# Kernel optimization log

Hardware: AMD Instinct MI355X
Metric: run time of the kernel (lower is better)

Reference implementation:

```python
import jax, jax.numpy as jnp
import numpy as np

B, S, DIM, HID = 2, 256, 128, 128
EPS = 1e-5

def _ln(t, w, b):
    mu = jnp.mean(t, axis=-1, keepdims=True)
    var = jnp.mean(jnp.square(t - mu), axis=-1, keepdims=True)
    return (t - mu) * jax.lax.rsqrt(var + EPS) * w + b

def setup_inputs() -> dict:
    key = jax.random.key(0)
    ks = jax.random.split(key, 8)
    sc = 1.0 / np.sqrt(DIM)
    return {
        "x": jax.random.normal(ks[0], (B, S, S, DIM), dtype=jnp.float32),
        "mask": jax.random.uniform(ks[1], (B, S, S), dtype=jnp.float32),
        "norm_w": jnp.ones((DIM,), jnp.float32),
        "norm_b": jnp.zeros((DIM,), jnp.float32),
        "w_left": jax.random.uniform(ks[2], (HID, DIM), jnp.float32, -sc, sc),
        "w_right": jax.random.uniform(ks[3], (HID, DIM), jnp.float32, -sc, sc),
        "w_lg": jax.random.uniform(ks[4], (HID, DIM), jnp.float32, -sc, sc),
        "w_rg": jax.random.uniform(ks[5], (HID, DIM), jnp.float32, -sc, sc),
        "w_og": jax.random.uniform(ks[6], (HID, DIM), jnp.float32, -sc, sc),
        "out_norm_w": jnp.ones((HID,), jnp.float32),
        "out_norm_b": jnp.zeros((HID,), jnp.float32),
        "w_out": jax.random.uniform(ks[7], (DIM, HID), jnp.float32, -1.0 / np.sqrt(HID), 1.0 / np.sqrt(HID)),
    }

def reference(x, mask, norm_w, norm_b, w_left, w_right, w_lg, w_rg, w_og,
              out_norm_w, out_norm_b, w_out):
    xn = _ln(x, norm_w, norm_b)                      # [B,S,S,D]
    m = mask[..., None]                              # [B,S,S,1]
    left = (xn @ w_left.T) * m * jax.nn.sigmoid(xn @ w_lg.T)    # [B,S,S,H]
    right = (xn @ w_right.T) * m * jax.nn.sigmoid(xn @ w_rg.T)  # [B,S,S,H]
    out_gate = jax.nn.sigmoid(xn @ w_og.T)
    # torch: permute to [B,H,S,S], bf16 bmm, permute back -> out[b,i,j,h] = sum_k L[b,i,k,h]*R[b,j,k,h]
    out = jnp.einsum("bikh,bjkh->bijh",
                     left.astype(jnp.bfloat16), right.astype(jnp.bfloat16),
                     preferred_element_type=jnp.float32)
    out = out.astype(jnp.bfloat16).astype(jnp.float32)
    out = _ln(out, out_norm_w, out_norm_b) * out_gate
    return out @ w_out.T                             # [B,S,S,D]
```

## Files before the change

### kernel.cpp

```cpp
#include <hip/hip_runtime.h>


#define SS 256
#define DD 128
#define HH 128

typedef __attribute__((ext_vector_type(8))) short bf16x8;
typedef __attribute__((ext_vector_type(4))) short bf16x4;
typedef __attribute__((ext_vector_type(4))) float f32x4;

__device__ __forceinline__ unsigned short f2b(float f) {
  unsigned u = __builtin_bit_cast(unsigned, f);
  u = (u + 0x7FFFu + ((u >> 16) & 1u)) >> 16;
  return (unsigned short)u;
}
__device__ __forceinline__ float b2f(unsigned short h) {
  return __builtin_bit_cast(float, ((unsigned)h) << 16);
}
__device__ __forceinline__ float sigmoidf_(float x) {
  return 1.0f / (1.0f + expf(-x));
}

__global__ __launch_bounds__(1024) void k_cvt(
    const float* __restrict__ s0, const float* __restrict__ s1,
    const float* __restrict__ s2, const float* __restrict__ s3,
    const float* __restrict__ s4, const float* __restrict__ s5,
    unsigned short* __restrict__ dst)
{
  int m = blockIdx.x >> 2;
  int e4 = (((blockIdx.x & 3) << 10) | threadIdx.x) << 2;
  const float* s = (m == 0) ? s0 : (m == 1) ? s1 : (m == 2) ? s2
                 : (m == 3) ? s3 : (m == 4) ? s4 : s5;
  f32x4 v = *(const f32x4*)(s + e4);
  bf16x4 r;
  #pragma unroll
  for (int i = 0; i < 4; ++i) r[i] = (short)f2b(v[i]);
  *(bf16x4*)(dst + m * 16384 + e4) = r;
}

__global__ __launch_bounds__(256, 4) void k_stage1(
    const float* __restrict__ x, const float* __restrict__ mask,
    const float* __restrict__ nw, const float* __restrict__ nb,
    const unsigned short* __restrict__ wb,
    unsigned short* __restrict__ Lt, unsigned short* __restrict__ Rt,
    unsigned short* __restrict__ og)
{
  __shared__ unsigned short xnS[64][136];
  __shared__ unsigned short oS[128][72];
  __shared__ float maskS[64];

  const int tid  = threadIdx.x;
  const int wave = tid >> 6, lane = tid & 63;
  const int quad = lane >> 4, l16 = lane & 15;
  const int r0 = blockIdx.x * 64;
  const int bq = r0 >> 16, iq = (r0 >> 8) & 255, j0 = r0 & 255;

  if (tid < 64) maskS[tid] = mask[r0 + tid];

  const float w0 = nw[lane], w1 = nw[lane + 64];
  const float b0 = nb[lane], b1 = nb[lane + 64];
  float v0a[16], v1a[16];
  #pragma unroll
  for (int rr = 0; rr < 16; ++rr) {
    const float* xr = x + (size_t)(r0 + wave * 16 + rr) * DD;
    v0a[rr] = xr[lane];
    v1a[rr] = xr[lane + 64];
  }
  #pragma unroll
  for (int rr = 0; rr < 16; ++rr) {
    int r = wave * 16 + rr;
    float v0 = v0a[rr], v1 = v1a[rr];
    float s = v0 + v1;
    #pragma unroll
    for (int o = 32; o; o >>= 1) s += __shfl_xor(s, o);
    float mu = s * (1.0f / 128.0f);
    float d0 = v0 - mu, d1 = v1 - mu;
    float q = d0 * d0 + d1 * d1;
    #pragma unroll
    for (int o = 32; o; o >>= 1) q += __shfl_xor(q, o);
    float rs = rsqrtf(q * (1.0f / 128.0f) + 1e-5f);
    xnS[r][lane]      = f2b(d0 * rs * w0 + b0);
    xnS[r][lane + 64] = f2b(d1 * rs * w1 + b1);
  }
  __syncthreads();

  const int h0 = wave * 32;
  const int jl = quad * 4;

  auto coopStore = [&](unsigned short* dstBase) {
    int h = tid >> 1, half = tid & 1;
    const bf16x8* s = (const bf16x8*)&oS[h][half * 32];
    bf16x8* d = (bf16x8*)(dstBase +
        ((((size_t)bq * 128 + h) * 256 + iq) * 256 + j0 + half * 32));
    d[0] = s[0]; d[1] = s[1]; d[2] = s[2]; d[3] = s[3];
  };

  auto gatedCompute = [&](const unsigned short* __restrict__ Wv,
                          const unsigned short* __restrict__ Wg,
                          f32x4 (&aV)[4][2], f32x4 (&aG)[4][2]) {
    const unsigned short* pv = Wv + (h0 + l16) * 128 + quad * 8;
    const unsigned short* pg = Wg + (h0 + l16) * 128 + quad * 8;
    #pragma unroll
    for (int rt = 0; rt < 4; ++rt)
      #pragma unroll
      for (int n = 0; n < 2; ++n) {
        aV[rt][n] = f32x4{0.f, 0.f, 0.f, 0.f};
        aG[rt][n] = f32x4{0.f, 0.f, 0.f, 0.f};
      }
    bf16x8 bv[2], bg[2], bvn[2], bgn[2];
    #pragma unroll
    for (int n = 0; n < 2; ++n) {
      bv[n] = *(const bf16x8*)(pv + n * 2048);
      bg[n] = *(const bf16x8*)(pg + n * 2048);
    }
    #pragma unroll
    for (int kk = 0; kk < 4; ++kk) {
      if (kk < 3) {
        #pragma unroll
        for (int n = 0; n < 2; ++n) {
          bvn[n] = *(const bf16x8*)(pv + n * 2048 + (kk + 1) * 32);
          bgn[n] = *(const bf16x8*)(pg + n * 2048 + (kk + 1) * 32);
        }
      }
      #pragma unroll
      for (int rt = 0; rt < 4; ++rt) {
        bf16x8 a = *(const bf16x8*)&xnS[rt * 16 + l16][kk * 32 + quad * 8];
        #pragma unroll
        for (int n = 0; n < 2; ++n) {
          aG[rt][n] = __builtin_amdgcn_mfma_f32_16x16x32_bf16(a, bg[n], aG[rt][n], 0, 0, 0);
          aV[rt][n] = __builtin_amdgcn_mfma_f32_16x16x32_bf16(a, bv[n], aV[rt][n], 0, 0, 0);
        }
      }
      #pragma unroll
      for (int n = 0; n < 2; ++n) { bv[n] = bvn[n]; bg[n] = bgn[n]; }
    }
  };

  auto gatedEpilogue = [&](f32x4 (&aV)[4][2], f32x4 (&aG)[4][2]) {
    #pragma unroll
    for (int rt = 0; rt < 4; ++rt)
      #pragma unroll
      for (int n = 0; n < 2; ++n) {
        bf16x4 p;
        #pragma unroll
        for (int rg = 0; rg < 4; ++rg) {
          float g = sigmoidf_(aG[rt][n][rg]);
          p[rg] = (short)f2b(aV[rt][n][rg] * maskS[rt * 16 + jl + rg] * g);
        }
        *(bf16x4*)&oS[h0 + n * 16 + l16][rt * 16 + jl] = p;
      }
  };

  f32x4 aV[4][2], aG[4][2];

  gatedCompute(wb + 0 * 16384, wb + 2 * 16384, aV, aG);
  gatedEpilogue(aV, aG);
  __syncthreads();
  coopStore(Lt);
  gatedCompute(wb + 1 * 16384, wb + 3 * 16384, aV, aG);
  __syncthreads();
  gatedEpilogue(aV, aG);
  __syncthreads();
  coopStore(Rt);

  {
    const unsigned short* po = wb + 4 * 16384 + (h0 + l16) * 128 + quad * 8;
    f32x4 aO[4][2];
    #pragma unroll
    for (int rt = 0; rt < 4; ++rt)
      #pragma unroll
      for (int n = 0; n < 2; ++n) aO[rt][n] = f32x4{0.f, 0.f, 0.f, 0.f};
    bf16x8 bo[2], bon[2];
    #pragma unroll
    for (int n = 0; n < 2; ++n) bo[n] = *(const bf16x8*)(po + n * 2048);
    #pragma unroll
    for (int kk = 0; kk < 4; ++kk) {
      if (kk < 3) {
        #pragma unroll
        for (int n = 0; n < 2; ++n)
          bon[n] = *(const bf16x8*)(po + n * 2048 + (kk + 1) * 32);
      }
      #pragma unroll
      for (int rt = 0; rt < 4; ++rt) {
        bf16x8 a = *(const bf16x8*)&xnS[rt * 16 + l16][kk * 32 + quad * 8];
        #pragma unroll
        for (int n = 0; n < 2; ++n)
          aO[rt][n] = __builtin_amdgcn_mfma_f32_16x16x32_bf16(bo[n], a, aO[rt][n], 0, 0, 0);
      }
      #pragma unroll
      for (int n = 0; n < 2; ++n) bo[n] = bon[n];
    }
    __syncthreads();
    unsigned short* ogS = &oS[0][0];
    #pragma unroll
    for (int rt = 0; rt < 4; ++rt)
      #pragma unroll
      for (int n = 0; n < 2; ++n) {
        bf16x4 p;
        #pragma unroll
        for (int rg = 0; rg < 4; ++rg)
          p[rg] = (short)f2b(sigmoidf_(aO[rt][n][rg]));
        *(bf16x4*)&ogS[(rt * 16 + l16) * 136 + h0 + n * 16 + quad * 4] = p;
      }
  }
  __syncthreads();
  {
    int j = tid >> 2, qq = tid & 3;
    const unsigned short* ogS = &oS[0][0];
    const bf16x8* sp = (const bf16x8*)&ogS[j * 136 + qq * 32];
    bf16x8* d = (bf16x8*)(og + (size_t)(r0 + j) * HH + qq * 32);
    d[0] = sp[0]; d[1] = sp[1]; d[2] = sp[2]; d[3] = sp[3];
  }
}

__global__ __launch_bounds__(256, 4) void k_stage2(
    const unsigned short* __restrict__ Lt, const unsigned short* __restrict__ Rt,
    unsigned short* __restrict__ Tt)
{
  __shared__ unsigned short As[128][72];
  __shared__ unsigned short Bs[128][72];

  const int tid  = threadIdx.x;
  const int wave = tid >> 6, lane = tid & 63;
  const int quad = lane >> 4, l16 = lane & 15;

  const int w   = blockIdx.y * 4 + blockIdx.x;
  const int grp = w >> 4;
  const int xcd = w & 7;
  const int jt  = (w >> 3) & 1;
  const int pid = grp * 8 + xcd;
  const int bh  = pid >> 1;
  const int it  = pid & 1;

  const unsigned short* A  = Lt + (size_t)bh * 65536 + it * 128 * 256;
  const unsigned short* Bp = Rt + (size_t)bh * 65536 + jt * 128 * 256;

  f32x4 acc[2][8];
  #pragma unroll
  for (int mt = 0; mt < 2; ++mt)
    #pragma unroll
    for (int nt = 0; nt < 8; ++nt) acc[mt][nt] = f32x4{0.f, 0.f, 0.f, 0.f};

  const int srow = tid >> 3, sc8 = tid & 7;

  bf16x8 ra[4], rb[4];
  #pragma unroll
  for (int i = 0; i < 4; ++i) {
    ra[i] = *(const bf16x8*)(A  + (i * 32 + srow) * 256 + sc8 * 8);
    rb[i] = *(const bf16x8*)(Bp + (i * 32 + srow) * 256 + sc8 * 8);
  }

  #pragma unroll
  for (int ks = 0; ks < 4; ++ks) {
    #pragma unroll
    for (int i = 0; i < 4; ++i) {
      *(bf16x8*)&As[i * 32 + srow][sc8 * 8] = ra[i];
      *(bf16x8*)&Bs[i * 32 + srow][sc8 * 8] = rb[i];
    }
    __syncthreads();
    if (ks < 3) {
      #pragma unroll
      for (int i = 0; i < 4; ++i) {
        ra[i] = *(const bf16x8*)(A  + (i * 32 + srow) * 256 + (ks + 1) * 64 + sc8 * 8);
        rb[i] = *(const bf16x8*)(Bp + (i * 32 + srow) * 256 + (ks + 1) * 64 + sc8 * 8);
      }
    }
    #pragma unroll
    for (int k2 = 0; k2 < 2; ++k2) {
      int ko = k2 * 32 + quad * 8;
      bf16x8 r0f = *(const bf16x8*)&Bs[wave * 32 + l16][ko];
      bf16x8 r1f = *(const bf16x8*)&Bs[wave * 32 + 16 + l16][ko];
      #pragma unroll
      for (int nt = 0; nt < 8; ++nt) {
        bf16x8 lf = *(const bf16x8*)&As[nt * 16 + l16][ko];
        acc[0][nt] = __builtin_amdgcn_mfma_f32_16x16x32_bf16(r0f, lf, acc[0][nt], 0, 0, 0);
        acc[1][nt] = __builtin_amdgcn_mfma_f32_16x16x32_bf16(r1f, lf, acc[1][nt], 0, 0, 0);
      }
    }
    __syncthreads();
  }

  unsigned short* C = Tt + (size_t)bh * 65536 + it * 128 * 256 + jt * 128;
  #pragma unroll
  for (int mt = 0; mt < 2; ++mt)
    #pragma unroll
    for (int nt = 0; nt < 8; ++nt) {
      bf16x4 p;
      #pragma unroll
      for (int rg = 0; rg < 4; ++rg) p[rg] = (short)f2b(acc[mt][nt][rg]);
      *(bf16x4*)&C[(nt * 16 + l16) * 256 + wave * 32 + mt * 16 + quad * 4] = p;
    }
}

__global__ __launch_bounds__(256, 4) void k_stage3(
    const unsigned short* __restrict__ Tt, const unsigned short* __restrict__ og,
    const float* __restrict__ onw, const float* __restrict__ onb,
    const unsigned short* __restrict__ wbO, float* __restrict__ out)
{
  __shared__ unsigned short tS[128][72];
  __shared__ unsigned short vS[64][136];
  __shared__ float onwS[128], onbS[128];

  const int tid  = threadIdx.x;
  const int wave = tid >> 6, lane = tid & 63;
  const int quad = lane >> 4, l16 = lane & 15;
  const int r0 = blockIdx.x * 64;
  const int bq = r0 >> 16, iq = (r0 >> 8) & 255, j0 = r0 & 255;
  const int jw = wave * 16;

  const int jE = jw + (lane >> 2), hq = lane & 3;
  bf16x8 gpre[4];
  {
    const unsigned short* ogp = og + (size_t)(r0 + jE) * HH + hq * 32;
    #pragma unroll
    for (int c = 0; c < 4; ++c) gpre[c] = *(const bf16x8*)(ogp + c * 8);
  }

  if (tid < 128) { onwS[tid] = onw[tid]; onbS[tid] = onb[tid]; }

  {
    int h = tid >> 1, half = tid & 1;
    int g = (h >> 5) & 3;
    const bf16x8* s = (const bf16x8*)(Tt +
        ((((size_t)bq * 128 + h) * 256 + iq) * 256 + j0 + half * 32));
    #pragma unroll
    for (int c = 0; c < 4; ++c)
      *(bf16x8*)&tS[h][((half * 4 + c) ^ g) << 3] = s[c];
  }
  __syncthreads();

  {
    int j  = jw + (lane & 15);
    int g2 = (lane >> 4) & 3;
    int hb = (lane >> 4) * 32;
    int jc = (((j >> 3) ^ g2) << 3) | (j & 7);
    #pragma unroll
    for (int c = 0; c < 4; ++c) {
      bf16x8 t;
      #pragma unroll
      for (int e = 0; e < 8; ++e) t[e] = (short)tS[hb + c * 8 + e][jc];
      *(bf16x8*)&vS[j][hb + c * 8] = t;
    }
  }
  asm volatile("s_waitcnt lgkmcnt(0)" ::: "memory");

  float mu, rs;
  {
    int j = jw + ((lane & 31) >> 1), h0 = (lane & 1) * 64;
    float s = 0.f, q = 0.f;
    #pragma unroll
    for (int c = 0; c < 8; ++c) {
      bf16x8 v8 = *(const bf16x8*)&vS[j][h0 + c * 8];
      #pragma unroll
      for (int e = 0; e < 8; ++e) {
        float v = b2f((unsigned short)v8[e]);
        s += v; q += v * v;
      }
    }
    s += __shfl_xor(s, 1);
    q += __shfl_xor(q, 1);
    mu = s * (1.0f / 128.0f);
    float var = q * (1.0f / 128.0f) - mu * mu;
    rs = rsqrtf(var + 1e-5f);
  }
  mu = __shfl(mu, (jE - jw) << 1);
  rs = __shfl(rs, (jE - jw) << 1);

  {
    unsigned short* vp = &vS[jE][hq * 32];
    #pragma unroll
    for (int c = 0; c < 4; ++c) {
      bf16x8 tv = *(bf16x8*)&vp[c * 8];
      bf16x8 gv = gpre[c];
      bf16x8 r;
      #pragma unroll
      for (int e = 0; e < 8; ++e) {
        int hh = hq * 32 + c * 8 + e;
        float v = (b2f((unsigned short)tv[e]) - mu) * rs * onwS[hh] + onbS[hh];
        r[e] = (short)f2b(v * b2f((unsigned short)gv[e]));
      }
      *(bf16x8*)&vp[c * 8] = r;
    }
  }
  asm volatile("s_waitcnt lgkmcnt(0)" ::: "memory");

  f32x4 acc[8];
  #pragma unroll
  for (int nt = 0; nt < 8; ++nt) acc[nt] = f32x4{0.f, 0.f, 0.f, 0.f};
  #pragma unroll
  for (int kk = 0; kk < 4; ++kk) {
    bf16x8 xv = *(const bf16x8*)&vS[jw + l16][kk * 32 + quad * 8];
    #pragma unroll
    for (int nt = 0; nt < 8; ++nt) {
      bf16x8 wv = *(const bf16x8*)(wbO + (nt * 16 + l16) * 128 + kk * 32 + quad * 8);
      acc[nt] = __builtin_amdgcn_mfma_f32_16x16x32_bf16(wv, xv, acc[nt], 0, 0, 0);
    }
  }
  #pragma unroll
  for (int nt = 0; nt < 8; ++nt)
    *(f32x4*)&out[(size_t)(r0 + jw + l16) * DD + nt * 16 + quad * 4] = acc[nt];
}

extern "C" void kernel_launch(void* const* d_in, const int* in_sizes, int n_in,
                              void* d_out, int out_size, void* d_ws, size_t ws_size,
                              hipStream_t stream)
{
  const float* x    = (const float*)d_in[0];
  const float* mask = (const float*)d_in[1];
  const float* nw   = (const float*)d_in[2];
  const float* nb   = (const float*)d_in[3];
  const float* wL   = (const float*)d_in[4];
  const float* wR   = (const float*)d_in[5];
  const float* wLG  = (const float*)d_in[6];
  const float* wRG  = (const float*)d_in[7];
  const float* wOG  = (const float*)d_in[8];
  const float* onw  = (const float*)d_in[9];
  const float* onb  = (const float*)d_in[10];
  const float* wO   = (const float*)d_in[11];

  char* ws = (char*)d_ws;
  unsigned short* wb = (unsigned short*)ws;
  unsigned short* og = (unsigned short*)(ws + (1 << 18));
  unsigned short* Lt = (unsigned short*)(ws + (1 << 18) + 1 * (size_t)(1 << 25));
  unsigned short* Rt = (unsigned short*)(ws + (1 << 18) + 2 * (size_t)(1 << 25));
  unsigned short* Tt = (unsigned short*)(ws + (1 << 18) + 3 * (size_t)(1 << 25));

  k_cvt<<<24, 1024, 0, stream>>>(wL, wR, wLG, wRG, wOG, wO, wb);
  k_stage1<<<2048, 256, 0, stream>>>(x, mask, nw, nb, wb, Lt, Rt, og);
  k_stage2<<<dim3(4, 256), 256, 0, stream>>>(Lt, Rt, Tt);
  k_stage3<<<2048, 256, 0, stream>>>(Tt, og, onw, onb, wb + 5 * 16384, (float*)d_out);
}
```

Before: 267.8 us.

## Fuse triangle bmm with output layernorm, gating and projection into one kernel

Replaces the separate batched-matmul kernel and the output LN/gate/projection kernel with one fused kernel. Each workgroup computes a 16x16 (i,j) tile across all 128 hidden channels using MFMA, fragments loaded straight from global memory, and keeps the bf16 result in a swizzled LDS buffer. It then applies layernorm, gating and the output projection in place. This removes the Tt intermediate round trip through HBM and one launch, but drops the LDS staging and reuse of L/R tiles, so L and R are re-read per tile, and it runs at lower occupancy with a large LDS footprint.

```diff
diff --git a/kernel.cpp b/kernel.cpp
--- a/kernel.cpp
+++ b/kernel.cpp
@@ -213,192 +213,124 @@
   }
 }
 
-__global__ __launch_bounds__(256, 4) void k_stage2(
+__global__ __launch_bounds__(256, 2) void k_fused(
     const unsigned short* __restrict__ Lt, const unsigned short* __restrict__ Rt,
-    unsigned short* __restrict__ Tt)
+    const unsigned short* __restrict__ og,
+    const float* __restrict__ onw, const float* __restrict__ onb,
+    const unsigned short* __restrict__ wbO, float* __restrict__ out)
 {
-  __shared__ unsigned short As[128][72];
-  __shared__ unsigned short Bs[128][72];
+  __shared__ unsigned short vvF[256 * 136];
+  __shared__ float onwS[128], onbS[128];
 
   const int tid  = threadIdx.x;
   const int wave = tid >> 6, lane = tid & 63;
   const int quad = lane >> 4, l16 = lane & 15;
 
-  const int w   = blockIdx.y * 4 + blockIdx.x;
-  const int grp = w >> 4;
-  const int xcd = w & 7;
-  const int jt  = (w >> 3) & 1;
-  const int pid = grp * 8 + xcd;
-  const int bh  = pid >> 1;
-  const int it  = pid & 1;
-
-  const unsigned short* A  = Lt + (size_t)bh * 65536 + it * 128 * 256;
-  const unsigned short* Bp = Rt + (size_t)bh * 65536 + jt * 128 * 256;
-
-  f32x4 acc[2][8];
-  #pragma unroll
-  for (int mt = 0; mt < 2; ++mt)
-    #pragma unroll
-    for (int nt = 0; nt < 8; ++nt) acc[mt][nt] = f32x4{0.f, 0.f, 0.f, 0.f};
-
-  const int srow = tid >> 3, sc8 = tid & 7;
-
-  bf16x8 ra[4], rb[4];
-  #pragma unroll
-  for (int i = 0; i < 4; ++i) {
-    ra[i] = *(const bf16x8*)(A  + (i * 32 + srow) * 256 + sc8 * 8);
-    rb[i] = *(const bf16x8*)(Bp + (i * 32 + srow) * 256 + sc8 * 8);
-  }
-
-  #pragma unroll
-  for (int ks = 0; ks < 4; ++ks) {
-    #pragma unroll
-    for (int i = 0; i < 4; ++i) {
-      *(bf16x8*)&As[i * 32 + srow][sc8 * 8] = ra[i];
-      *(bf16x8*)&Bs[i * 32 + srow][sc8 * 8] = rb[i];
-    }
-    __syncthreads();
-    if (ks < 3) {
-      #pragma unroll
-      for (int i = 0; i < 4; ++i) {
-        ra[i] = *(const bf16x8*)(A  + (i * 32 + srow) * 256 + (ks + 1) * 64 + sc8 * 8);
-        rb[i] = *(const bf16x8*)(Bp + (i * 32 + srow) * 256 + (ks + 1) * 64 + sc8 * 8);
-      }
-    }
-    #pragma unroll
-    for (int k2 = 0; k2 < 2; ++k2) {
-      int ko = k2 * 32 + quad * 8;
-      bf16x8 r0f = *(const bf16x8*)&Bs[wave * 32 + l16][ko];
-      bf16x8 r1f = *(const bf16x8*)&Bs[wave * 32 + 16 + l16][ko];
-      #pragma unroll
-      for (int nt = 0; nt < 8; ++nt) {
-        bf16x8 lf = *(const bf16x8*)&As[nt * 16 + l16][ko];
-        acc[0][nt] = __builtin_amdgcn_mfma_f32_16x16x32_bf16(r0f, lf, acc[0][nt], 0, 0, 0);
-        acc[1][nt] = __builtin_amdgcn_mfma_f32_16x16x32_bf16(r1f, lf, acc[1][nt], 0, 0, 0);
-      }
-    }
-    __syncthreads();
-  }
-
-  unsigned short* C = Tt + (size_t)bh * 65536 + it * 128 * 256 + jt * 128;
-  #pragma unroll
-  for (int mt = 0; mt < 2; ++mt)
-    #pragma unroll
-    for (int nt = 0; nt < 8; ++nt) {
-      bf16x4 p;
-      #pragma unroll
-      for (int rg = 0; rg < 4; ++rg) p[rg] = (short)f2b(acc[mt][nt][rg]);
-      *(bf16x4*)&C[(nt * 16 + l16) * 256 + wave * 32 + mt * 16 + quad * 4] = p;
-    }
-}
-
-__global__ __launch_bounds__(256, 4) void k_stage3(
-    const unsigned short* __restrict__ Tt, const unsigned short* __restrict__ og,
-    const float* __restrict__ onw, const float* __restrict__ onb,
-    const unsigned short* __restrict__ wbO, float* __restrict__ out)
-{
-  __shared__ unsigned short tS[128][72];
-  __shared__ unsigned short vS[64][136];
-  __shared__ float onwS[128], onbS[128];
-
-  const int tid  = threadIdx.x;
-  const int wave = tid >> 6, lane = tid & 63;
-  const int quad = lane >> 4, l16 = lane & 15;
-  const int r0 = blockIdx.x * 64;
-  const int bq = r0 >> 16, iq = (r0 >> 8) & 255, j0 = r0 & 255;
-  const int jw = wave * 16;
-
-  const int jE = jw + (lane >> 2), hq = lane & 3;
-  bf16x8 gpre[4];
-  {
-    const unsigned short* ogp = og + (size_t)(r0 + jE) * HH + hq * 32;
-    #pragma unroll
-    for (int c = 0; c < 4; ++c) gpre[c] = *(const bf16x8*)(ogp + c * 8);
-  }
+  const int wg   = blockIdx.x;
+  const int orig = (wg & 7) * 64 + (wg >> 3);
+  const int b  = orig >> 8;
+  const int i0 = ((orig >> 4) & 15) * 16;
+  const int j0 = (orig & 15) * 16;
 
   if (tid < 128) { onwS[tid] = onw[tid]; onbS[tid] = onb[tid]; }
 
-  {
-    int h = tid >> 1, half = tid & 1;
-    int g = (h >> 5) & 3;
-    const bf16x8* s = (const bf16x8*)(Tt +
-        ((((size_t)bq * 128 + h) * 256 + iq) * 256 + j0 + half * 32));
-    #pragma unroll
-    for (int c = 0; c < 4; ++c)
-      *(bf16x8*)&tS[h][((half * 4 + c) ^ g) << 3] = s[c];
-  }
-  __syncthreads();
-
-  {
-    int j  = jw + (lane & 15);
-    int g2 = (lane >> 4) & 3;
-    int hb = (lane >> 4) * 32;
-    int jc = (((j >> 3) ^ g2) << 3) | (j & 7);
-    #pragma unroll
-    for (int c = 0; c < 4; ++c) {
-      bf16x8 t;
-      #pragma unroll
-      for (int e = 0; e < 8; ++e) t[e] = (short)tS[hb + c * 8 + e][jc];
-      *(bf16x8*)&vS[j][hb + c * 8] = t;
-    }
-  }
-  asm volatile("s_waitcnt lgkmcnt(0)" ::: "memory");
+  const unsigned short* Lp = Lt + ((size_t)(b * 128 + wave * 32) * 256 + (i0 + l16)) * 256 + quad * 8;
+  const unsigned short* Rp = Rt + ((size_t)(b * 128 + wave * 32) * 256 + (j0 + l16)) * 256 + quad * 8;
+
+  #pragma unroll 1
+  for (int g8 = 0; g8 < 4; ++g8) {
+    bf16x8 pk[4];
+    #pragma unroll
+    for (int hg = 0; hg < 8; ++hg) {
+      bf16x8 lf[8], rf[8];
+      #pragma unroll
+      for (int kk = 0; kk < 8; ++kk) {
+        rf[kk] = *(const bf16x8*)(Rp + kk * 32);
+        lf[kk] = *(const bf16x8*)(Lp + kk * 32);
+      }
+      f32x4 acc = f32x4{0.f, 0.f, 0.f, 0.f};
+      #pragma unroll
+      for (int kk = 0; kk < 8; ++kk)
+        acc = __builtin_amdgcn_mfma_f32_16x16x32_bf16(rf[kk], lf[kk], acc, 0, 0, 0);
+      #pragma unroll
+      for (int rg = 0; rg < 4; ++rg) pk[rg][hg] = (short)f2b(acc[rg]);
+      Lp += 65536; Rp += 65536;
+    }
+    const int h0 = wave * 32 + g8 * 8;
+    #pragma unroll
+    for (int rg = 0; rg < 4; ++rg) {
+      int row = l16 * 16 + quad * 4 + rg;
+      *(bf16x8*)&vvF[row * 136 + ((((h0 >> 2) ^ ((row >> 3) & 14)) << 2))] = pk[rg];
+    }
+  }
+  __syncthreads();
+
+  const int iL = tid >> 4, jL = tid & 15;
+  const unsigned short* ogp = og +
+      ((size_t)b * 65536 + (size_t)(i0 + iL) * 256 + (j0 + jL)) * 128;
+  bf16x8 gpre[16];
+  #pragma unroll
+  for (int c = 0; c < 16; ++c) gpre[c] = *(const bf16x8*)(ogp + c * 8);
 
   float mu, rs;
   {
-    int j = jw + ((lane & 31) >> 1), h0 = (lane & 1) * 64;
-    float s = 0.f, q = 0.f;
+    float sl = 0.f, ql = 0.f, sh = 0.f, qh = 0.f;
     #pragma unroll
     for (int c = 0; c < 8; ++c) {
-      bf16x8 v8 = *(const bf16x8*)&vS[j][h0 + c * 8];
-      #pragma unroll
-      for (int e = 0; e < 8; ++e) {
-        float v = b2f((unsigned short)v8[e]);
-        s += v; q += v * v;
-      }
-    }
-    s += __shfl_xor(s, 1);
-    q += __shfl_xor(q, 1);
+      bf16x8 v8 = *(const bf16x8*)&vvF[tid * 136 + (((c * 2) ^ ((tid >> 3) & 14)) << 2)];
+      #pragma unroll
+      for (int e = 0; e < 8; ++e) { float v = b2f((unsigned short)v8[e]); sl += v; ql += v * v; }
+    }
+    #pragma unroll
+    for (int c = 8; c < 16; ++c) {
+      bf16x8 v8 = *(const bf16x8*)&vvF[tid * 136 + (((c * 2) ^ ((tid >> 3) & 14)) << 2)];
+      #pragma unroll
+      for (int e = 0; e < 8; ++e) { float v = b2f((unsigned short)v8[e]); sh += v; qh += v * v; }
+    }
+    float s = sl + sh, q = ql + qh;
     mu = s * (1.0f / 128.0f);
     float var = q * (1.0f / 128.0f) - mu * mu;
     rs = rsqrtf(var + 1e-5f);
   }
-  mu = __shfl(mu, (jE - jw) << 1);
-  rs = __shfl(rs, (jE - jw) << 1);
-
-  {
-    unsigned short* vp = &vS[jE][hq * 32];
-    #pragma unroll
-    for (int c = 0; c < 4; ++c) {
-      bf16x8 tv = *(bf16x8*)&vp[c * 8];
-      bf16x8 gv = gpre[c];
-      bf16x8 r;
-      #pragma unroll
-      for (int e = 0; e < 8; ++e) {
-        int hh = hq * 32 + c * 8 + e;
-        float v = (b2f((unsigned short)tv[e]) - mu) * rs * onwS[hh] + onbS[hh];
-        r[e] = (short)f2b(v * b2f((unsigned short)gv[e]));
-      }
-      *(bf16x8*)&vp[c * 8] = r;
-    }
+
+  #pragma unroll
+  for (int c = 0; c < 16; ++c) {
+    unsigned short* vp = &vvF[tid * 136 + (((c * 2) ^ ((tid >> 3) & 14)) << 2)];
+    bf16x8 tv = *(bf16x8*)vp;
+    bf16x8 gv = gpre[c];
+    bf16x8 r;
+    #pragma unroll
+    for (int e = 0; e < 8; ++e) {
+      int hh = c * 8 + e;
+      float v = (b2f((unsigned short)tv[e]) - mu) * rs * onwS[hh] + onbS[hh];
+      r[e] = (short)f2b(v * b2f((unsigned short)gv[e]));
+    }
+    *(bf16x8*)vp = r;
   }
   asm volatile("s_waitcnt lgkmcnt(0)" ::: "memory");
 
-  f32x4 acc[8];
-  #pragma unroll
-  for (int nt = 0; nt < 8; ++nt) acc[nt] = f32x4{0.f, 0.f, 0.f, 0.f};
-  #pragma unroll
-  for (int kk = 0; kk < 4; ++kk) {
-    bf16x8 xv = *(const bf16x8*)&vS[jw + l16][kk * 32 + quad * 8];
-    #pragma unroll
-    for (int nt = 0; nt < 8; ++nt) {
-      bf16x8 wv = *(const bf16x8*)(wbO + (nt * 16 + l16) * 128 + kk * 32 + quad * 8);
-      acc[nt] = __builtin_amdgcn_mfma_f32_16x16x32_bf16(wv, xv, acc[nt], 0, 0, 0);
-    }
-  }
-  #pragma unroll
-  for (int nt = 0; nt < 8; ++nt)
-    *(f32x4*)&out[(size_t)(r0 + jw + l16) * DD + nt * 16 + quad * 4] = acc[nt];
+  #pragma unroll
+  for (int ii = 0; ii < 4; ++ii) {
+    const int iO = wave * 4 + ii;
+    f32x4 acc[8];
+    #pragma unroll
+    for (int nt = 0; nt < 8; ++nt) acc[nt] = f32x4{0.f, 0.f, 0.f, 0.f};
+    #pragma unroll
+    for (int kk = 0; kk < 4; ++kk) {
+      int row = iO * 16 + l16;
+      bf16x8 xv = *(const bf16x8*)&vvF[row * 136 +
+          ((((kk * 32 + quad * 8) >> 2) ^ ((row >> 3) & 14)) << 2)];
+      #pragma unroll
+      for (int nt = 0; nt < 8; ++nt) {
+        bf16x8 wv = *(const bf16x8*)(wbO + (nt * 16 + l16) * 128 + kk * 32 + quad * 8);
+        acc[nt] = __builtin_amdgcn_mfma_f32_16x16x32_bf16(wv, xv, acc[nt], 0, 0, 0);
+      }
+    }
+    float* op = out + ((size_t)(b * 256 + i0 + iO) * 256 + j0 + l16) * 128 + quad * 4;
+    #pragma unroll
+    for (int nt = 0; nt < 8; ++nt)
+      *(f32x4*)(op + nt * 16) = acc[nt];
+  }
 }
 
 extern "C" void kernel_launch(void* const* d_in, const int* in_sizes, int n_in,
@@ -423,10 +355,8 @@
   unsigned short* og = (unsigned short*)(ws + (1 << 18));
   unsigned short* Lt = (unsigned short*)(ws + (1 << 18) + 1 * (size_t)(1 << 25));
   unsigned short* Rt = (unsigned short*)(ws + (1 << 18) + 2 * (size_t)(1 << 25));
-  unsigned short* Tt = (unsigned short*)(ws + (1 << 18) + 3 * (size_t)(1 << 25));
 
   k_cvt<<<24, 1024, 0, stream>>>(wL, wR, wLG, wRG, wOG, wO, wb);
   k_stage1<<<2048, 256, 0, stream>>>(x, mask, nw, nb, wb, Lt, Rt, og);
-  k_stage2<<<dim3(4, 256), 256, 0, stream>>>(Lt, Rt, Tt);
-  k_stage3<<<2048, 256, 0, stream>>>(Tt, og, onw, onb, wb + 5 * 16384, (float*)d_out);
-}
+  k_fused<<<512, 256, 0, stream>>>(Lt, Rt, og, onw, onb, wb + 5 * 16384, (float*)d_out);
+}
```

Measured after the change: 351.7 us. +31.3%, slower.
